# Performance work log

Hardware: AMD Instinct MI355X
Metric: run time of the kernel (lower is better)

## Reference

```python
import jax, jax.numpy as jnp
import numpy as np

T, B, I, H = 512, 64, 1024, 1024
SIGMA = 0.01

def setup_inputs() -> dict:
    key = jax.random.key(0)
    k1, k2, k3 = jax.random.split(key, 3)
    X = jax.random.normal(k1, (T, B, I), dtype=jnp.float32)
    W_xh = jax.random.normal(k2, (I, H), dtype=jnp.float32) * SIGMA
    W_hh = jax.random.normal(k3, (H, H), dtype=jnp.float32) * SIGMA
    b_h = jnp.zeros((H,), dtype=jnp.float32)
    return {"X": X, "W_xh": W_xh, "W_hh": W_hh, "b_h": b_h}

def reference(X, W_xh, W_hh, b_h):
    # Precompute input projection for all timesteps in one big GEMM: [T,B,I]@[I,H]
    Xp = jnp.einsum('tbi,ih->tbh', X, W_xh) + b_h
    state0 = jnp.zeros((X.shape[1], W_hh.shape[0]), dtype=X.dtype)

    def step(state, xp_t):
        new_state = jnp.tanh(xp_t + state @ W_hh)
        return new_state, new_state

    final_state, outputs = jax.lax.scan(step, state0, Xp)
    return outputs, final_state
```

## Files before the change

### kernel.cpp

```cpp
#include <hip/hip_runtime.h>
#include <hip/hip_bf16.h>
#include <stdint.h>

typedef short bf16x8 __attribute__((ext_vector_type(8)));
typedef float f32x4  __attribute__((ext_vector_type(4)));
typedef unsigned int u32x4 __attribute__((ext_vector_type(4)));

static __device__ __forceinline__ unsigned short bf16_rne(float f) {
    unsigned u = __builtin_bit_cast(unsigned, f);
    unsigned r = u + 0x7fffu + ((u >> 16) & 1u);
    return (unsigned short)(r >> 16);
}
static __device__ __forceinline__ float bf16tof(unsigned short h) {
    unsigned u = ((unsigned)h) << 16;
    return __builtin_bit_cast(float, u);
}

__global__ __launch_bounds__(256) void k_transpose(const float* __restrict__ W,
                                                   unsigned short* __restrict__ Wt) {
    __shared__ float tile[64][65];
    int bx = blockIdx.x & 15, by = blockIdx.x >> 4;
    int n0 = bx * 64, k0 = by * 64;
    int tx = threadIdx.x & 63, ty = threadIdx.x >> 6;
#pragma unroll
    for (int p = 0; p < 16; ++p) {
        int r = p * 4 + ty;
        tile[r][tx] = W[(size_t)(k0 + r) * 1024 + n0 + tx];
    }
    __syncthreads();
#pragma unroll
    for (int p = 0; p < 16; ++p) {
        int r = p * 4 + ty;
        Wt[(size_t)(n0 + r) * 1024 + k0 + tx] = bf16_rne(tile[tx][r]);
    }
}

#define LDA 80

__global__ __launch_bounds__(256) void k_xpgemm(const float* __restrict__ X,
                                                const unsigned short* __restrict__ Wt,
                                                const float* __restrict__ bh,
                                                unsigned short* __restrict__ Xp) {
    __shared__ __align__(16) unsigned char ldsA[128 * LDA];
    __shared__ __align__(16) unsigned char ldsB[128 * LDA];
    int p = blockIdx.x;
    int lo = (p & 7) * 256 + (p >> 3);
    int mt = lo >> 3, nt = lo & 7;
    int m0 = mt * 128, n0 = nt * 128;
    int tid = threadIdx.x;
    int lane = tid & 63, wid = tid >> 6;
    int wr = wid >> 1, wc = wid & 1;
    int mw = wr * 64, nw = wc * 64;
    int l15 = lane & 15, kg = lane >> 4;

    f32x4 acc[4][4] = {};
    int arow = tid >> 3, as = tid & 7;
    int brow = tid >> 2, bs = tid & 3;

    for (int kt = 0; kt < 32; ++kt) {
#pragma unroll
        for (int pp = 0; pp < 4; ++pp) {
            int r = pp * 32 + arow;
            const float4 v = *(const float4*)(X + (size_t)(m0 + r) * 1024 + kt * 32 + as * 4);
            unsigned lo32 = ((unsigned)bf16_rne(v.y) << 16) | bf16_rne(v.x);
            unsigned hi32 = ((unsigned)bf16_rne(v.w) << 16) | bf16_rne(v.z);
            *(uint2*)(ldsA + r * LDA + as * 8) = make_uint2(lo32, hi32);
        }
#pragma unroll
        for (int pp = 0; pp < 2; ++pp) {
            int r = pp * 64 + brow;
            uint4 v = *(const uint4*)(Wt + (size_t)(n0 + r) * 1024 + kt * 32 + bs * 8);
            *(uint4*)(ldsB + r * LDA + bs * 16) = v;
        }
        __syncthreads();
        bf16x8 af[4];
#pragma unroll
        for (int i = 0; i < 4; ++i)
            af[i] = *(const bf16x8*)(ldsA + (mw + 16 * i + l15) * LDA + kg * 16);
#pragma unroll
        for (int j = 0; j < 4; ++j) {
            bf16x8 bfj = *(const bf16x8*)(ldsB + (nw + 16 * j + l15) * LDA + kg * 16);
#pragma unroll
            for (int i = 0; i < 4; ++i)
                acc[i][j] = __builtin_amdgcn_mfma_f32_16x16x32_bf16(af[i], bfj, acc[i][j], 0, 0, 0);
        }
        __syncthreads();
    }
#pragma unroll
    for (int j = 0; j < 4; ++j) {
        int col = n0 + nw + 16 * j + l15;
        float bias = bh[col];
#pragma unroll
        for (int i = 0; i < 4; ++i) {
            int rb = m0 + mw + 16 * i + kg * 4;
#pragma unroll
            for (int r = 0; r < 4; ++r)
                Xp[(size_t)(rb + r) * 1024 + col] = bf16_rne(acc[i][j][r] + bias);
        }
    }
}

#define SB0 __builtin_amdgcn_sched_barrier(0)
#define WV0 asm volatile("s_waitcnt vmcnt(0)" ::: "memory")

template<int S> static __device__ __forceinline__ void ld16s(u32x4& d, uint64_t a) {
    if constexpr (S) asm volatile("global_load_dwordx4 %0, %1, off sc0" : "=v"(d) : "v"(a) : "memory");
    else             asm volatile("global_load_dwordx4 %0, %1, off sc1" : "=v"(d) : "v"(a) : "memory");
}
template<int S> static __device__ __forceinline__ void sths(uint64_t a, unsigned v) {
    if constexpr (S) asm volatile("global_store_short %0, %1, off sc0" :: "v"(a), "v"(v) : "memory");
    else             asm volatile("global_store_short %0, %1, off sc1" :: "v"(a), "v"(v) : "memory");
}
template<int S> static __device__ __forceinline__ void stds(uint64_t a, unsigned v) {
    if constexpr (S) asm volatile("global_store_dword %0, %1, off sc0" :: "v"(a), "v"(v) : "memory");
    else             asm volatile("global_store_dword %0, %1, off sc1" :: "v"(a), "v"(v) : "memory");
}
template<int S> static __device__ __forceinline__ unsigned lddw_wait(uint64_t a) {
    unsigned f;
    if constexpr (S) asm volatile("global_load_dword %0, %1, off sc0\n\ts_waitcnt vmcnt(0)" : "=v"(f) : "v"(a) : "memory");
    else             asm volatile("global_load_dword %0, %1, off sc1\n\ts_waitcnt vmcnt(0)" : "=v"(f) : "v"(a) : "memory");
    return f;
}
static __device__ __forceinline__ void st_sys(uint64_t a, unsigned v) {
    asm volatile("global_store_dword %0, %1, off sc0 sc1" :: "v"(a), "v"(v) : "memory");
}
static __device__ __forceinline__ unsigned ld_sys_wait(uint64_t a) {
    unsigned f;
    asm volatile("global_load_dword %0, %1, off sc0 sc1\n\ts_waitcnt vmcnt(0)" : "=v"(f) : "v"(a) : "memory");
    return f;
}

template<int S>
static __device__ __forceinline__ void scan_main(
    const float* __restrict__ Whh, const unsigned short* __restrict__ Xp,
    unsigned short* __restrict__ hbuf, unsigned* __restrict__ flags,
    float* __restrict__ out, unsigned char* lds, int chain, int mypos, int tid) {

    const int lane = tid & 63, wid = tid >> 6;
    const int l15 = lane & 15, kg = lane >> 4;
    const int jj = mypos * 128 + wid * 16 + l15;
    const int gr = chain * 16 + kg * 4;

    bf16x8 w[32];
#pragma unroll
    for (int i = 0; i < 32; ++i)
#pragma unroll
        for (int e = 0; e < 8; ++e)
            w[i][e] = (short)bf16_rne(Whh[(size_t)(i * 32 + kg * 8 + e) * 1024 + jj]);

    const uint64_t hb_c = (uint64_t)hbuf + (uint64_t)chain * 65536;
    const uint64_t fl_c = (uint64_t)flags + (uint64_t)chain * 64;
    const uint64_t fpoll = fl_c + (uint64_t)(lane & 7) * 4;
    const uint64_t myflag = fl_c + (uint64_t)mypos * 4;
    const int crow = tid >> 5;
    const uint64_t crd = hb_c + (uint64_t)crow * 2048 + (tid & 31) * 64;
    unsigned char* ldsw = lds + (tid & 31) * 1296 + crow * 80;
    const unsigned char* lrd = lds + l15 * 80 + kg * 16;
    const uint64_t hwr = hb_c + (uint64_t)(kg * 4) * 2048 + (uint64_t)jj * 2;
    const unsigned short* xpb = Xp + (size_t)gr * 1024 + jj;

    float hv[4];

    for (int t = 0; t < 512; ++t) {
        if (t > 0 && wid == 0) {
            unsigned tt = (unsigned)t;
            for (;;) {
                unsigned f = lddw_wait<S>(fpoll);
                if (__all(f >= tt)) break;
            }
        }
        __syncthreads();

        u32x4 c0, c1, c2, c3;
        const uint64_t ca = crd + (uint64_t)(t & 1) * 32768;
        ld16s<S>(c0, ca); ld16s<S>(c1, ca + 16); ld16s<S>(c2, ca + 32); ld16s<S>(c3, ca + 48);
        unsigned short xr[4];
#pragma unroll
        for (int r = 0; r < 4; ++r)
            xr[r] = xpb[(size_t)t * 65536 + r * 1024];
        WV0; SB0;
        *(u32x4*)(ldsw)      = c0; *(u32x4*)(ldsw + 16) = c1;
        *(u32x4*)(ldsw + 32) = c2; *(u32x4*)(ldsw + 48) = c3;
        __syncthreads();

        f32x4 a0 = {0.f, 0.f, 0.f, 0.f}, a1 = {0.f, 0.f, 0.f, 0.f};
        f32x4 a2 = {0.f, 0.f, 0.f, 0.f}, a3 = {0.f, 0.f, 0.f, 0.f};
#pragma unroll
        for (int ks = 0; ks < 8; ++ks) {
            a0 = __builtin_amdgcn_mfma_f32_16x16x32_bf16(
                *(const bf16x8*)(lrd + (4 * ks + 0) * 1296), w[4 * ks + 0], a0, 0, 0, 0);
            a1 = __builtin_amdgcn_mfma_f32_16x16x32_bf16(
                *(const bf16x8*)(lrd + (4 * ks + 1) * 1296), w[4 * ks + 1], a1, 0, 0, 0);
            a2 = __builtin_amdgcn_mfma_f32_16x16x32_bf16(
                *(const bf16x8*)(lrd + (4 * ks + 2) * 1296), w[4 * ks + 2], a2, 0, 0, 0);
            a3 = __builtin_amdgcn_mfma_f32_16x16x32_bf16(
                *(const bf16x8*)(lrd + (4 * ks + 3) * 1296), w[4 * ks + 3], a3, 0, 0, 0);
        }
        f32x4 acc = (a0 + a1) + (a2 + a3);

        unsigned hb4[4];
#pragma unroll
        for (int r = 0; r < 4; ++r) {
            float z = acc[r] + bf16tof(xr[r]);
            z = fminf(fmaxf(z, -15.f), 15.f);
            float e = __expf(2.f * z);
            float v = (e - 1.f) / (e + 1.f);
            hv[r] = v;
            hb4[r] = (unsigned)bf16_rne(v);
        }

        if (t < 511) {
            const uint64_t hn = hwr + (uint64_t)((t + 1) & 1) * 32768;
            sths<S>(hn, hb4[0]); sths<S>(hn + 2048, hb4[1]);
            sths<S>(hn + 4096, hb4[2]); sths<S>(hn + 6144, hb4[3]);
            WV0;
        }
        __syncthreads();
        if (t < 511 && tid == 0)
            stds<S>(myflag, (unsigned)(t + 1));

#pragma unroll
        for (int r = 0; r < 4; ++r)
            out[(size_t)(t * 64 + gr + r) * 1024 + jj] = hv[r];
    }
#pragma unroll
    for (int r = 0; r < 4; ++r)
        out[(size_t)33554432 + (size_t)(gr + r) * 1024 + jj] = hv[r];
}

__global__ __launch_bounds__(512) void k_scan(const float* __restrict__ Whh,
                                              const unsigned short* __restrict__ Xp,
                                              unsigned short* __restrict__ hbuf,
                                              unsigned int* flags,
                                              unsigned int* aux,
                                              float* __restrict__ out) {
    __shared__ __align__(16) unsigned char lds[32 * 1296];
    const int wgid = blockIdx.x, tid = threadIdx.x;
    const int lane = tid & 63, wid = tid >> 6;
    const int c8 = wgid & 7;
    if (c8 >= 4) return;
    const int chain = c8, mypos = wgid >> 3;
    const int windex = mypos * 4 + chain;
    const uint64_t A = (uint64_t)aux;
    const uint64_t F = (uint64_t)flags;

    unsigned xcc;
    asm volatile("s_getreg_b32 %0, hwreg(20, 0, 32)" : "=s"(xcc));
    xcc &= 7u;
    if (tid == 0) {
        if (mypos == 0) {
            uint64_t tm;
            asm volatile("s_memtime %0" : "=s"(tm));
            st_sys(F + 960 + (uint64_t)chain * 4, ((unsigned)tm ^ (unsigned)(tm >> 32)) | 1u);
        }
        st_sys(A + (uint64_t)windex * 4, xcc);
        WV0;
        st_sys(A + 128 + (uint64_t)windex * 4, 1u);
    }
    {
        uint64_t p = A + 128 + (uint64_t)(chain + 4 * (lane & 7)) * 4;
        for (;;) { unsigned f = ld_sys_wait(p); if (__all(f == 1u)) break; }
    }
    unsigned mapok;
    {
        unsigned x = ld_sys_wait(A + (uint64_t)(chain + 4 * (lane & 7)) * 4);
        unsigned x0 = (unsigned)__shfl((int)x, 0);
        mapok = __all(x == x0) ? 1u : 0u;
    }
    const unsigned nonce = ld_sys_wait(F + 960 + (uint64_t)chain * 4);

    const int l15 = lane & 15, kg = lane >> 4;
    const uint64_t hwr0 = (uint64_t)hbuf + (uint64_t)chain * 65536 +
                          (uint64_t)(kg * 4) * 2048 +
                          (uint64_t)(mypos * 128 + wid * 16 + l15) * 2;
    if (mapok) {
#pragma unroll
        for (int par = 0; par < 2; ++par)
#pragma unroll
            for (int r = 0; r < 4; ++r)
                sths<1>(hwr0 + (uint64_t)par * 32768 + (uint64_t)r * 2048, 0u);
        if (tid == 0) {
            stds<1>(F + (uint64_t)chain * 64 + (uint64_t)mypos * 4, 0u);
            stds<1>(A + 640 + (uint64_t)windex * 4, 0u);
        }
        WV0;
    }
    __syncthreads();
    if (tid == 0) st_sys(A + 256 + (uint64_t)windex * 4, 1u);
    {
        uint64_t p = A + 256 + (uint64_t)(chain + 4 * (lane & 7)) * 4;
        for (;;) { unsigned f = ld_sys_wait(p); if (__all(f == 1u)) break; }
    }

    unsigned localok = mapok;
    if (mapok) {
        if (tid == 0) stds<1>(A + 640 + (uint64_t)windex * 4, nonce ^ (unsigned)windex);
        uint64_t p = A + 640 + (uint64_t)(chain + 4 * (lane & 7)) * 4;
        unsigned expv = nonce ^ (unsigned)(chain + 4 * (lane & 7));
        int ok = 0;
        for (int it = 0; it < 5000; ++it) {
            unsigned f = lddw_wait<1>(p);
            if (__all(f == expv)) { ok = 1; break; }
        }
        localok = (unsigned)ok;
    }
    if (tid == 0) {
        st_sys(A + 384 + (uint64_t)windex * 4, localok ? 1u : 2u);
        WV0;
        st_sys(A + 512 + (uint64_t)windex * 4, 1u);
    }
    {
        uint64_t p = A + 512 + (uint64_t)(chain + 4 * (lane & 7)) * 4;
        for (;;) { unsigned f = ld_sys_wait(p); if (__all(f == 1u)) break; }
    }
    unsigned v = ld_sys_wait(A + 384 + (uint64_t)(chain + 4 * (lane & 7)) * 4);
    const int FAST = __all(v == 1u) ? 1 : 0;
    __syncthreads();

    if (FAST) scan_main<1>(Whh, Xp, hbuf, flags, out, lds, chain, mypos, tid);
    else      scan_main<0>(Whh, Xp, hbuf, flags, out, lds, chain, mypos, tid);
}

extern "C" void kernel_launch(void* const* d_in, const int* in_sizes, int n_in,
                              void* d_out, int out_size, void* d_ws, size_t ws_size,
                              hipStream_t stream) {
    const float* X   = (const float*)d_in[0];
    const float* Wxh = (const float*)d_in[1];
    const float* Whh = (const float*)d_in[2];
    const float* bh  = (const float*)d_in[3];
    float* out = (float*)d_out;
    unsigned char* ws = (unsigned char*)d_ws;

    unsigned short* Wt    = (unsigned short*)(ws);
    unsigned short* Xp    = (unsigned short*)(ws + 2097152);
    unsigned short* hbuf  = (unsigned short*)(ws + 69206016);
    unsigned int*   flags = (unsigned int*)(ws + 69468160);
    unsigned int*   aux   = (unsigned int*)(ws + 69468416);

    hipMemsetAsync(ws + 69206016, 0, 263168, stream);
    hipLaunchKernelGGL(k_transpose, dim3(256), dim3(256), 0, stream, Wxh, Wt);
    hipLaunchKernelGGL(k_xpgemm, dim3(2048), dim3(256), 0, stream, X, Wt, bh, Xp);
    hipLaunchKernelGGL(k_scan, dim3(64), dim3(512), 0, stream, Whh, Xp, hbuf, flags, aux, out);
}
```

Measured before the change: 2.258 ms.

## Transpose MFMA operands for contiguous per-lane outputs and vectorized stores

Swaps the MFMA A/B operands so each lane owns one batch row and four consecutive hidden columns. The hidden-state writes then become a single 8-byte store, the Xp loads a single dwordx2 prefetched one step ahead, and the output writes a single dwordx4. Every wave now polls the flags itself, which removes one __syncthreads per step. The LDS layout for the staged hidden state is reorganized to match, which adds more concurrent flag polling traffic in exchange for fewer and wider memory operations on the serial critical path.

Result: faster. 2.099 ms (-7.1%).

```diff
diff --git a/kernel.cpp b/kernel.cpp
--- a/kernel.cpp
+++ b/kernel.cpp
@@ -5,6 +5,7 @@
 typedef short bf16x8 __attribute__((ext_vector_type(8)));
 typedef float f32x4  __attribute__((ext_vector_type(4)));
 typedef unsigned int u32x4 __attribute__((ext_vector_type(4)));
+typedef unsigned int u32x2 __attribute__((ext_vector_type(2)));
 
 static __device__ __forceinline__ unsigned short bf16_rne(float f) {
     unsigned u = __builtin_bit_cast(unsigned, f);
@@ -107,9 +108,9 @@
     if constexpr (S) asm volatile("global_load_dwordx4 %0, %1, off sc0" : "=v"(d) : "v"(a) : "memory");
     else             asm volatile("global_load_dwordx4 %0, %1, off sc1" : "=v"(d) : "v"(a) : "memory");
 }
-template<int S> static __device__ __forceinline__ void sths(uint64_t a, unsigned v) {
-    if constexpr (S) asm volatile("global_store_short %0, %1, off sc0" :: "v"(a), "v"(v) : "memory");
-    else             asm volatile("global_store_short %0, %1, off sc1" :: "v"(a), "v"(v) : "memory");
+template<int S> static __device__ __forceinline__ void st8s(uint64_t a, u32x2 v) {
+    if constexpr (S) asm volatile("global_store_dwordx2 %0, %1, off sc0" :: "v"(a), "v"(v) : "memory");
+    else             asm volatile("global_store_dwordx2 %0, %1, off sc1" :: "v"(a), "v"(v) : "memory");
 }
 template<int S> static __device__ __forceinline__ void stds(uint64_t a, unsigned v) {
     if constexpr (S) asm volatile("global_store_dword %0, %1, off sc0" :: "v"(a), "v"(v) : "memory");
@@ -138,46 +139,43 @@
 
     const int lane = tid & 63, wid = tid >> 6;
     const int l15 = lane & 15, kg = lane >> 4;
-    const int jj = mypos * 128 + wid * 16 + l15;
-    const int gr = chain * 16 + kg * 4;
+    const int jt = mypos * 128 + wid * 16;
+    const int b  = chain * 16 + l15;
+    const int jl = jt + kg * 4;
 
     bf16x8 w[32];
 #pragma unroll
     for (int i = 0; i < 32; ++i)
 #pragma unroll
         for (int e = 0; e < 8; ++e)
-            w[i][e] = (short)bf16_rne(Whh[(size_t)(i * 32 + kg * 8 + e) * 1024 + jj]);
+            w[i][e] = (short)bf16_rne(Whh[(size_t)(i * 32 + kg * 8 + e) * 1024 + jt + l15]);
 
     const uint64_t hb_c = (uint64_t)hbuf + (uint64_t)chain * 65536;
     const uint64_t fl_c = (uint64_t)flags + (uint64_t)chain * 64;
-    const uint64_t fpoll = fl_c + (uint64_t)(lane & 7) * 4;
+    const uint64_t fpoll = fl_c + (uint64_t)wid * 4;
     const uint64_t myflag = fl_c + (uint64_t)mypos * 4;
-    const int crow = tid >> 5;
-    const uint64_t crd = hb_c + (uint64_t)crow * 2048 + (tid & 31) * 64;
-    unsigned char* ldsw = lds + (tid & 31) * 1296 + crow * 80;
-    const unsigned char* lrd = lds + l15 * 80 + kg * 16;
-    const uint64_t hwr = hb_c + (uint64_t)(kg * 4) * 2048 + (uint64_t)jj * 2;
-    const unsigned short* xpb = Xp + (size_t)gr * 1024 + jj;
-
-    float hv[4];
+
+    const uint64_t crd = hb_c + (uint64_t)(lane >> 2) * 2048 + wid * 256 + (lane & 3) * 64;
+    unsigned char* ldsw = lds + (lane >> 2) * 2064 + wid * 256 + (lane & 3) * 64;
+    const unsigned char* lrd = lds + l15 * 2064 + kg * 16;
+
+    const uint64_t hwr  = hb_c + (uint64_t)l15 * 2048 + (uint64_t)jl * 2;
+    const uint64_t xpb  = (uint64_t)Xp + ((uint64_t)b * 1024 + jl) * 2;
+    const uint64_t outb = (uint64_t)out + ((uint64_t)b * 1024 + jl) * 4;
+
+    u32x2 xr;
+    asm volatile("global_load_dwordx2 %0, %1, off" : "=v"(xr) : "v"(xpb) : "memory");
+
+    f32x4 hv = {0.f, 0.f, 0.f, 0.f};
 
     for (int t = 0; t < 512; ++t) {
-        if (t > 0 && wid == 0) {
+        if (t > 0) {
             unsigned tt = (unsigned)t;
-            for (;;) {
-                unsigned f = lddw_wait<S>(fpoll);
-                if (__all(f >= tt)) break;
-            }
-        }
-        __syncthreads();
-
+            for (;;) { unsigned f = lddw_wait<S>(fpoll); if (__all(f >= tt)) break; }
+        }
         u32x4 c0, c1, c2, c3;
         const uint64_t ca = crd + (uint64_t)(t & 1) * 32768;
         ld16s<S>(c0, ca); ld16s<S>(c1, ca + 16); ld16s<S>(c2, ca + 32); ld16s<S>(c3, ca + 48);
-        unsigned short xr[4];
-#pragma unroll
-        for (int r = 0; r < 4; ++r)
-            xr[r] = xpb[(size_t)t * 65536 + r * 1024];
         WV0; SB0;
         *(u32x4*)(ldsw)      = c0; *(u32x4*)(ldsw + 16) = c1;
         *(u32x4*)(ldsw + 32) = c2; *(u32x4*)(ldsw + 48) = c3;
@@ -188,44 +186,48 @@
 #pragma unroll
         for (int ks = 0; ks < 8; ++ks) {
             a0 = __builtin_amdgcn_mfma_f32_16x16x32_bf16(
-                *(const bf16x8*)(lrd + (4 * ks + 0) * 1296), w[4 * ks + 0], a0, 0, 0, 0);
+                w[4 * ks + 0], *(const bf16x8*)(lrd + (4 * ks + 0) * 64), a0, 0, 0, 0);
             a1 = __builtin_amdgcn_mfma_f32_16x16x32_bf16(
-                *(const bf16x8*)(lrd + (4 * ks + 1) * 1296), w[4 * ks + 1], a1, 0, 0, 0);
+                w[4 * ks + 1], *(const bf16x8*)(lrd + (4 * ks + 1) * 64), a1, 0, 0, 0);
             a2 = __builtin_amdgcn_mfma_f32_16x16x32_bf16(
-                *(const bf16x8*)(lrd + (4 * ks + 2) * 1296), w[4 * ks + 2], a2, 0, 0, 0);
+                w[4 * ks + 2], *(const bf16x8*)(lrd + (4 * ks + 2) * 64), a2, 0, 0, 0);
             a3 = __builtin_amdgcn_mfma_f32_16x16x32_bf16(
-                *(const bf16x8*)(lrd + (4 * ks + 3) * 1296), w[4 * ks + 3], a3, 0, 0, 0);
+                w[4 * ks + 3], *(const bf16x8*)(lrd + (4 * ks + 3) * 64), a3, 0, 0, 0);
         }
         f32x4 acc = (a0 + a1) + (a2 + a3);
 
-        unsigned hb4[4];
+        float xpf[4] = { bf16tof((unsigned short)(xr[0] & 0xffffu)),
+                         bf16tof((unsigned short)(xr[0] >> 16)),
+                         bf16tof((unsigned short)(xr[1] & 0xffffu)),
+                         bf16tof((unsigned short)(xr[1] >> 16)) };
+        unsigned hb16[4];
 #pragma unroll
         for (int r = 0; r < 4; ++r) {
-            float z = acc[r] + bf16tof(xr[r]);
+            float z = acc[r] + xpf[r];
             z = fminf(fmaxf(z, -15.f), 15.f);
             float e = __expf(2.f * z);
             float v = (e - 1.f) / (e + 1.f);
             hv[r] = v;
-            hb4[r] = (unsigned)bf16_rne(v);
+            hb16[r] = (unsigned)bf16_rne(v);
         }
 
         if (t < 511) {
-            const uint64_t hn = hwr + (uint64_t)((t + 1) & 1) * 32768;
-            sths<S>(hn, hb4[0]); sths<S>(hn + 2048, hb4[1]);
-            sths<S>(hn + 4096, hb4[2]); sths<S>(hn + 6144, hb4[3]);
+            u32x2 hh = { hb16[0] | (hb16[1] << 16), hb16[2] | (hb16[3] << 16) };
+            st8s<S>(hwr + (uint64_t)((t + 1) & 1) * 32768, hh);
             WV0;
         }
         __syncthreads();
-        if (t < 511 && tid == 0)
-            stds<S>(myflag, (unsigned)(t + 1));
-
-#pragma unroll
-        for (int r = 0; r < 4; ++r)
-            out[(size_t)(t * 64 + gr + r) * 1024 + jj] = hv[r];
-    }
-#pragma unroll
-    for (int r = 0; r < 4; ++r)
-        out[(size_t)33554432 + (size_t)(gr + r) * 1024 + jj] = hv[r];
+        if (t < 511 && tid == 0) stds<S>(myflag, (unsigned)(t + 1));
+
+        if (t < 511)
+            asm volatile("global_load_dwordx2 %0, %1, off"
+                         : "=v"(xr) : "v"(xpb + (uint64_t)(t + 1) * 131072) : "memory");
+        asm volatile("global_store_dwordx4 %0, %1, off"
+                     :: "v"(outb + (uint64_t)t * 262144), "v"(hv) : "memory");
+    }
+    asm volatile("global_store_dwordx4 %0, %1, off"
+                 :: "v"((uint64_t)out + ((uint64_t)33554432 + (uint64_t)b * 1024 + jl) * 4),
+                    "v"(hv) : "memory");
 }
 
 __global__ __launch_bounds__(512) void k_scan(const float* __restrict__ Whh,
@@ -234,7 +236,7 @@
                                               unsigned int* flags,
                                               unsigned int* aux,
                                               float* __restrict__ out) {
-    __shared__ __align__(16) unsigned char lds[32 * 1296];
+    __shared__ __align__(16) unsigned char lds[16 * 2064];
     const int wgid = blockIdx.x, tid = threadIdx.x;
     const int lane = tid & 63, wid = tid >> 6;
     const int c8 = wgid & 7;
@@ -271,14 +273,14 @@
 
     const int l15 = lane & 15, kg = lane >> 4;
     const uint64_t hwr0 = (uint64_t)hbuf + (uint64_t)chain * 65536 +
-                          (uint64_t)(kg * 4) * 2048 +
-                          (uint64_t)(mypos * 128 + wid * 16 + l15) * 2;
+                          (uint64_t)l15 * 2048 +
+                          (uint64_t)(mypos * 128 + wid * 16 + kg * 4) * 2;
     if (mapok) {
 #pragma unroll
-        for (int par = 0; par < 2; ++par)
-#pragma unroll
-            for (int r = 0; r < 4; ++r)
-                sths<1>(hwr0 + (uint64_t)par * 32768 + (uint64_t)r * 2048, 0u);
+        for (int par = 0; par < 2; ++par) {
+            stds<1>(hwr0 + (uint64_t)par * 32768, 0u);
+            stds<1>(hwr0 + (uint64_t)par * 32768 + 4, 0u);
+        }
         if (tid == 0) {
             stds<1>(F + (uint64_t)chain * 64 + (uint64_t)mypos * 4, 0u);
             stds<1>(A + 640 + (uint64_t)windex * 4, 0u);
```
